# Performance work log

Measured on AMD Instinct MI355X. Metric: run time of the kernel, lower is better.

The kernel has to match this reference:

```python
import jax, jax.numpy as jnp
import numpy as np

B, T, HID = 4, 2048, 1024
H, DK, DV, K = 8, 64, 128, 4
EPS = 1e-5


def _dw_causal_conv(x, w, b):
    # x: (B,T,C), w: (C,1,K) depthwise, b: (C,). Causal: left-pad K-1.
    xt = jnp.transpose(x, (0, 2, 1))  # (B,C,T)
    y = jax.lax.conv_general_dilated(
        xt, w, window_strides=(1,), padding=[(K - 1, 0)],
        dimension_numbers=("NCH", "OIH", "NCH"), feature_group_count=x.shape[-1])
    y = y + b[None, :, None]
    return jnp.transpose(y, (0, 2, 1))  # (B,T,C)


def setup_inputs() -> dict:
    key = jax.random.key(0)
    ks = jax.random.split(key, 20)
    s = 0.02
    inp = {
        "x": jax.random.normal(ks[0], (B, T, HID), jnp.float32),
        "Wq": jax.random.normal(ks[1], (H * DK, HID), jnp.float32) * s,
        "Wk": jax.random.normal(ks[2], (H * DK, HID), jnp.float32) * s,
        "Wv": jax.random.normal(ks[3], (H * DV, HID), jnp.float32) * s,
        "Wa": jax.random.normal(ks[4], (H * DV, HID), jnp.float32) * s,
        "ba": jax.random.normal(ks[5], (H * DV,), jnp.float32) * s,
        "Wb": jax.random.normal(ks[6], (H, HID), jnp.float32) * s,
        "bb": jax.random.normal(ks[7], (H,), jnp.float32) * s,
        "Wg": jax.random.normal(ks[8], (H * DV, HID), jnp.float32) * s,
        "Wo": jax.random.normal(ks[9], (HID, H * DV), jnp.float32) * s,
        "qc_w": jax.random.normal(ks[10], (H * DK, 1, K), jnp.float32) * 0.3,
        "qc_b": jnp.zeros((H * DK,), jnp.float32),
        "kc_w": jax.random.normal(ks[11], (H * DK, 1, K), jnp.float32) * 0.3,
        "kc_b": jnp.zeros((H * DK,), jnp.float32),
        "vc_w": jax.random.normal(ks[12], (H * DV, 1, K), jnp.float32) * 0.3,
        "vc_b": jnp.zeros((H * DV,), jnp.float32),
        "ln_w": jnp.ones((DV,), jnp.float32),
        "ln_b": jnp.zeros((DV,), jnp.float32),
    }
    return inp


def _forward(x, Wq, Wk, Wv, Wa, ba, Wb, bb, Wg, Wo,
             qc_w, qc_b, kc_w, kc_b, vc_w, vc_b, ln_w, ln_b):
    b, t = x.shape[0], x.shape[1]
    scale = DK ** -0.5
    q = x @ Wq.T
    k = x @ Wk.T
    v = x @ Wv.T
    q = jax.nn.silu(_dw_causal_conv(q, qc_w, qc_b))
    k = jax.nn.silu(_dw_causal_conv(k, kc_w, kc_b))
    v = jax.nn.silu(_dw_causal_conv(v, vc_w, vc_b))
    q = q.reshape(b, t, H, DK)
    k = (k * scale).reshape(b, t, H, DK)
    v = v.reshape(b, t, H, DV)
    a = jax.nn.sigmoid(x @ Wa.T + ba).reshape(b, t, H, DV)
    beta = jax.nn.sigmoid(x @ Wb.T + bb)  # (B,T,H)

    # gated delta-rule recurrence over time; state S: (B,H,DK,DV)
    def step(S, ins):
        q_t, k_t, v_t, a_t, b_t = ins
        read = jnp.einsum("bhk,bhkv->bhv", k_t, S)          # (B,H,DV)
        err = read - v_t
        S = (a_t[:, :, None, :] * S
             - b_t[:, :, None, None] * k_t[..., None] * err[:, :, None, :])
        o_t = jnp.einsum("bhk,bhkv->bhv", q_t, S)
        return S, o_t

    to_tbh = lambda u: jnp.moveaxis(u, 1, 0)  # (T,B,H,...)
    S0 = jnp.zeros((b, H, DK, DV), x.dtype)
    _, o = jax.lax.scan(step, S0, (to_tbh(q), to_tbh(k), to_tbh(v),
                                   to_tbh(a), to_tbh(beta)))
    o = jnp.moveaxis(o, 0, 1)  # (B,T,H,DV)

    # LayerNorm over DV
    mu = jnp.mean(o, axis=-1, keepdims=True)
    var = jnp.mean((o - mu) ** 2, axis=-1, keepdims=True)
    o = (o - mu) * jax.lax.rsqrt(var + EPS) * ln_w + ln_b

    g = jax.nn.sigmoid(x @ Wg.T).reshape(b, t, H, DV)
    o = (o * g).reshape(b, t, H * DV)
    return o @ Wo.T


def reference(x, Wq, Wk, Wv, Wa, ba, Wb, bb, Wg, Wo,
              qc_w, qc_b, kc_w, kc_b, vc_w, vc_b, ln_w, ln_b):
    return _forward(x, Wq, Wk, Wv, Wa, ba, Wb, bb, Wg, Wo,
                    qc_w, qc_b, kc_w, kc_b, vc_w, vc_b, ln_w, ln_b)
```

## Files before the change

### kernel.cpp

```cpp
#include <hip/hip_runtime.h>
#include <hip/hip_bf16.h>
#include <cstdint>
#include <cstddef>

#define TDIM 2048
#define NH 8

using f32x4 = __attribute__((ext_vector_type(4))) float;
using s16x8 = __attribute__((ext_vector_type(8))) short;

__device__ __forceinline__ float sigm(float x) { return 1.0f / (1.0f + __expf(-x)); }

#define GLDS(gp, lp)                                                          \
    __builtin_amdgcn_global_load_lds(                                         \
        (const __attribute__((address_space(1))) void*)(gp),                  \
        (__attribute__((address_space(3))) void*)(lp), 16, 0, 0)
#define GLDS4(gp, lp)                                                         \
    __builtin_amdgcn_global_load_lds(                                         \
        (const __attribute__((address_space(1))) void*)(gp),                  \
        (__attribute__((address_space(3))) void*)(lp), 4, 0, 0)

template<int CTRL>
__device__ __forceinline__ float dpp_add(float x) {
    int p = __builtin_amdgcn_mov_dpp(__float_as_int(x), CTRL, 0xF, 0xF, true);
    return x + __int_as_float(p);
}
__device__ __forceinline__ float reduce16(float x) {
    x = dpp_add<0xB1>(x);
    x = dpp_add<0x4E>(x);
    x = dpp_add<0x141>(x);
    x = dpp_add<0x140>(x);
    return x;
}

__global__ __launch_bounds__(256) void pack_f32_bf16_kernel(
    const float* __restrict__ src, __hip_bfloat16* __restrict__ dst, int n4)
{
    int i = blockIdx.x * 256 + threadIdx.x;
    if (i >= n4) return;
    float4 v = *(const float4*)(src + (size_t)i * 4);
    size_t o = (size_t)i * 4;
    dst[o + 0] = __float2bfloat16(v.x);
    dst[o + 1] = __float2bfloat16(v.y);
    dst[o + 2] = __float2bfloat16(v.z);
    dst[o + 3] = __float2bfloat16(v.w);
}

__global__ __launch_bounds__(256) void pack_w_kernel(
    const float* __restrict__ Wq, const float* __restrict__ Wk,
    const float* __restrict__ Wv, const float* __restrict__ Wa,
    const float* __restrict__ Wb, const float* __restrict__ Wg,
    __hip_bfloat16* __restrict__ dst)
{
    int e = blockIdx.x * 256 + threadIdx.x;
    int r = e >> 10, c = e & 1023;
    float vv;
    if      (r <  512) vv = Wq[(size_t)r * 1024 + c];
    else if (r < 1024) vv = Wk[(size_t)(r -  512) * 1024 + c];
    else if (r < 2048) vv = Wv[(size_t)(r - 1024) * 1024 + c];
    else if (r < 3072) vv = Wa[(size_t)(r - 2048) * 1024 + c];
    else if (r < 3080) vv = Wb[(size_t)(r - 3072) * 1024 + c];
    else if (r < 4104) vv = Wg[(size_t)(r - 3080) * 1024 + c];
    else               vv = 0.0f;
    dst[e] = __float2bfloat16(vv);
}

__global__ __launch_bounds__(256) void gemm1_kernel(
    const __hip_bfloat16* __restrict__ A, const __hip_bfloat16* __restrict__ Bw,
    float* __restrict__ qraw, float* __restrict__ kraw, float* __restrict__ vraw,
    float* __restrict__ abuf, float* __restrict__ betab, float* __restrict__ gbuf,
    const float* __restrict__ ba, const float* __restrict__ bb)
{
    constexpr int Kd = 1024;
    __shared__ __attribute__((aligned(16))) __hip_bfloat16 At[128 * 32];
    __shared__ __attribute__((aligned(16))) __hip_bfloat16 Bt[128 * 32];
    __shared__ __attribute__((aligned(16))) float Ct[4][16 * 68];
    const int tid = threadIdx.x;
    const int mBase = blockIdx.x * 128;
    const int nBase = blockIdx.y * 128;
    const int wave = tid >> 6, lane = tid & 63;
    const int wm = (wave >> 1) * 64, wn = (wave & 1) * 64;
    const int quad = lane >> 4, l16 = lane & 15;

    f32x4 acc[4][4];
    for (int i = 0; i < 4; i++)
        for (int j = 0; j < 4; j++)
            for (int r = 0; r < 4; r++) acc[i][j][r] = 0.0f;

    const int srow = tid >> 2;
    const int skk = (tid & 3) * 8;
    const __hip_bfloat16* Ag = A + (size_t)(mBase + srow) * Kd + skk;
    const __hip_bfloat16* Bg = Bw + (size_t)(nBase + srow) * Kd + skk;
    __hip_bfloat16* Al = &At[srow * 32 + skk];
    __hip_bfloat16* Bl = &Bt[srow * 32 + skk];

    for (int k0 = 0; k0 < Kd; k0 += 32) {
        GLDS(Ag + k0, Al);
        GLDS(Ag + k0 + (size_t)64 * Kd, Al + 64 * 32);
        GLDS(Bg + k0, Bl);
        GLDS(Bg + k0 + (size_t)64 * Kd, Bl + 64 * 32);
        __syncthreads();
        s16x8 af[4], bfr[4];
#pragma unroll
        for (int i = 0; i < 4; i++)
            af[i] = *(const s16x8*)&At[(wm + i * 16 + l16) * 32 + quad * 8];
#pragma unroll
        for (int j = 0; j < 4; j++)
            bfr[j] = *(const s16x8*)&Bt[(wn + j * 16 + l16) * 32 + quad * 8];
#pragma unroll
        for (int i = 0; i < 4; i++)
#pragma unroll
            for (int j = 0; j < 4; j++)
                acc[i][j] = __builtin_amdgcn_mfma_f32_16x16x32_bf16(af[i], bfr[j], acc[i][j], 0, 0, 0);
        __syncthreads();
    }

    const int ncol = nBase + wn + l16 * 4;
    float* basep; size_t rstr; bool dosig = false; bool skip = false;
    float4 bias = make_float4(0.f, 0.f, 0.f, 0.f);
    if (ncol < 512)       { basep = qraw + ncol;          rstr = 512;  }
    else if (ncol < 1024) { basep = kraw + (ncol - 512);  rstr = 512;  }
    else if (ncol < 2048) { basep = vraw + (ncol - 1024); rstr = 1024; }
    else if (ncol < 3072) { basep = abuf + (ncol - 2048); rstr = 1024; dosig = true;
                            bias = *(const float4*)(ba + (ncol - 2048)); }
    else if (ncol < 3080) { basep = betab + (ncol - 3072); rstr = 8;   dosig = true;
                            bias = *(const float4*)(bb + (ncol - 3072)); }
    else if (ncol < 4104) { basep = gbuf + (ncol - 3080); rstr = 1024; dosig = true; }
    else                  { basep = gbuf; rstr = 0; skip = true; }

#pragma unroll
    for (int i = 0; i < 4; i++) {
#pragma unroll
        for (int j = 0; j < 4; j++)
#pragma unroll
            for (int r = 0; r < 4; r++)
                Ct[wave][(quad * 4 + r) * 68 + j * 16 + l16] = acc[i][j][r];
        __syncthreads();
#pragma unroll
        for (int p = 0; p < 4; p++) {
            int rr = p * 4 + quad;
            float4 val = *(const float4*)&Ct[wave][rr * 68 + l16 * 4];
            if (dosig) {
                val.x = sigm(val.x + bias.x);
                val.y = sigm(val.y + bias.y);
                val.z = sigm(val.z + bias.z);
                val.w = sigm(val.w + bias.w);
            }
            int m = mBase + wm + i * 16 + rr;
            if (!skip) *(float4*)(basep + (size_t)m * rstr) = val;
        }
        __syncthreads();
    }
}

__global__ __launch_bounds__(256) void gemm2_kernel(
    const __hip_bfloat16* __restrict__ A, const __hip_bfloat16* __restrict__ Bw,
    float* __restrict__ out)
{
    constexpr int Kd = 1024;
    __shared__ __attribute__((aligned(16))) __hip_bfloat16 At[128 * 32];
    __shared__ __attribute__((aligned(16))) __hip_bfloat16 Bt[128 * 32];
    __shared__ __attribute__((aligned(16))) float Ct[4][16 * 68];
    const int tid = threadIdx.x;
    const int mBase = blockIdx.x * 128;
    const int nBase = blockIdx.y * 128;
    const int wave = tid >> 6, lane = tid & 63;
    const int wm = (wave >> 1) * 64, wn = (wave & 1) * 64;
    const int quad = lane >> 4, l16 = lane & 15;

    f32x4 acc[4][4];
    for (int i = 0; i < 4; i++)
        for (int j = 0; j < 4; j++)
            for (int r = 0; r < 4; r++) acc[i][j][r] = 0.0f;

    const int srow = tid >> 2;
    const int skk = (tid & 3) * 8;
    const __hip_bfloat16* Ag = A + (size_t)(mBase + srow) * Kd + skk;
    const __hip_bfloat16* Bg = Bw + (size_t)(nBase + srow) * Kd + skk;
    __hip_bfloat16* Al = &At[srow * 32 + skk];
    __hip_bfloat16* Bl = &Bt[srow * 32 + skk];

    for (int k0 = 0; k0 < Kd; k0 += 32) {
        GLDS(Ag + k0, Al);
        GLDS(Ag + k0 + (size_t)64 * Kd, Al + 64 * 32);
        GLDS(Bg + k0, Bl);
        GLDS(Bg + k0 + (size_t)64 * Kd, Bl + 64 * 32);
        __syncthreads();
        s16x8 af[4], bfr[4];
#pragma unroll
        for (int i = 0; i < 4; i++)
            af[i] = *(const s16x8*)&At[(wm + i * 16 + l16) * 32 + quad * 8];
#pragma unroll
        for (int j = 0; j < 4; j++)
            bfr[j] = *(const s16x8*)&Bt[(wn + j * 16 + l16) * 32 + quad * 8];
#pragma unroll
        for (int i = 0; i < 4; i++)
#pragma unroll
            for (int j = 0; j < 4; j++)
                acc[i][j] = __builtin_amdgcn_mfma_f32_16x16x32_bf16(af[i], bfr[j], acc[i][j], 0, 0, 0);
        __syncthreads();
    }

    const int ncol = nBase + wn + l16 * 4;
    float* basep = out + ncol;
#pragma unroll
    for (int i = 0; i < 4; i++) {
#pragma unroll
        for (int j = 0; j < 4; j++)
#pragma unroll
            for (int r = 0; r < 4; r++)
                Ct[wave][(quad * 4 + r) * 68 + j * 16 + l16] = acc[i][j][r];
        __syncthreads();
#pragma unroll
        for (int p = 0; p < 4; p++) {
            int rr = p * 4 + quad;
            float4 val = *(const float4*)&Ct[wave][rr * 68 + l16 * 4];
            int m = mBase + wm + i * 16 + rr;
            *(float4*)(basep + (size_t)m * 1024) = val;
        }
        __syncthreads();
    }
}

__global__ __launch_bounds__(256) void conv_silu_fused_kernel(
    const float* __restrict__ qraw, const float* __restrict__ kraw,
    const float* __restrict__ vraw,
    const float* __restrict__ qw, const float* __restrict__ qb,
    const float* __restrict__ kw, const float* __restrict__ kb,
    const float* __restrict__ vw, const float* __restrict__ vb,
    float* __restrict__ qcb, float* __restrict__ kcb, float* __restrict__ vcb)
{
    int e = blockIdx.x * 256 + threadIdx.x;
    int c = e & 2047;
    int bt = e >> 11;
    int t = bt & (TDIM - 1);
    const float* src; float* dst; const float* w4; const float* bi;
    int C, cc; float scale = 1.0f;
    if (c < 512)       { src = qraw; dst = qcb; w4 = qw; bi = qb; C = 512;  cc = c; }
    else if (c < 1024) { src = kraw; dst = kcb; w4 = kw; bi = kb; C = 512;  cc = c - 512; scale = 0.125f; }
    else               { src = vraw; dst = vcb; w4 = vw; bi = vb; C = 1024; cc = c - 1024; }
    const float* wc = w4 + (size_t)cc * 4;
    const float* s = src + (size_t)bt * C + cc;
    float acc = bi[cc];
    acc = fmaf(s[0], wc[3], acc);
    if (t >= 1) acc = fmaf(s[-C], wc[2], acc);
    if (t >= 2) acc = fmaf(s[-2 * C], wc[1], acc);
    if (t >= 3) acc = fmaf(s[-3 * C], wc[0], acc);
    dst[(size_t)bt * C + cc] = acc * sigm(acc) * scale;
}

#define CH 32
#define NCHUNK (TDIM / CH)

#define SCAN_STAGE(BUF, T0) do {                                              \
    _Pragma("unroll") for (int j = 0; j < 8; j++) {                           \
        int flat = j * 64 + lane;                                             \
        int tt = flat >> 4, c4 = (flat & 15) * 4;                             \
        GLDS(kc + kqB + (size_t)((T0) + tt) * 512 + c4, &kL[BUF][j * 256]);   \
        GLDS(qc + kqB + (size_t)((T0) + tt) * 512 + c4, &qL[BUF][j * 256]);   \
    }                                                                         \
    _Pragma("unroll") for (int j = 0; j < 2; j++) {                           \
        int flat = j * 64 + lane;                                             \
        int tt = flat >> 2, c1 = flat & 3;                                    \
        GLDS4(vc + vaB + (size_t)((T0) + tt) * 1024 + c1, &vL[BUF][j * 64]);  \
        GLDS4(ab + vaB + (size_t)((T0) + tt) * 1024 + c1, &aL[BUF][j * 64]);  \
    }                                                                         \
    if (lane < CH)                                                            \
        GLDS4(betab + beB + (size_t)((T0) + lane) * 8, &bL[BUF][0]);          \
} while (0)

#define LOADOPS(BUF, TT, SL) do {                                             \
    kR[SL] = *(const float4*)&kL[BUF][(TT) * 64 + ks * 4];                    \
    qR[SL] = *(const float4*)&qL[BUF][(TT) * 64 + ks * 4];                    \
    vR[SL] = vL[BUF][(TT) * 4 + vi];                                          \
    aR[SL] = aL[BUF][(TT) * 4 + vi];                                          \
    bR[SL] = bL[BUF][TT];                                                     \
} while (0)

#define CSTEP(SL, TT) do {                                                    \
    const float4 kk = kR[SL];                                                 \
    const float4 qq = qR[SL];                                                 \
    const float AA = aR[SL], BB = bR[SL], VV = vR[SL];                        \
    float as0 = AA * S0, as1 = AA * S1, as2 = AA * S2, as3 = AA * S3;         \
    float bv = BB * VV;                                                       \
    float r0 = kk.x * S0, r1 = kk.y * S1;                                     \
    r0 = fmaf(kk.z, S2, r0); r1 = fmaf(kk.w, S3, r1);                         \
    float rr = reduce16(r0 + r1);                                             \
    float cc = fmaf(BB, rr, -bv);                                             \
    S0 = fmaf(-cc, kk.x, as0); float o0 = qq.x * S0;                          \
    S1 = fmaf(-cc, kk.y, as1); float o1 = qq.y * S1;                          \
    S2 = fmaf(-cc, kk.z, as2); o0 = fmaf(qq.z, S2, o0);                       \
    S3 = fmaf(-cc, kk.w, as3); o1 = fmaf(qq.w, S3, o1);                       \
    oacc[TT] = reduce16(o0 + o1);                                             \
} while (0)

__global__ __launch_bounds__(64) void scan_kernel(
    const float* __restrict__ qc, const float* __restrict__ kc,
    const float* __restrict__ vc, const float* __restrict__ ab,
    const float* __restrict__ betab, float* __restrict__ ob)
{
    __shared__ __attribute__((aligned(16))) float kL[2][CH * 64];
    __shared__ __attribute__((aligned(16))) float qL[2][CH * 64];
    __shared__ __attribute__((aligned(16))) float vL[2][CH * 4];
    __shared__ __attribute__((aligned(16))) float aL[2][CH * 4];
    __shared__ __attribute__((aligned(16))) float bL[2][CH];
    __shared__ __attribute__((aligned(16))) float oL[4 * CH];

    const int bid = blockIdx.x;
    const int bh = bid & 31, vg = bid >> 5;
    const int h = bh & 7, b = bh >> 3;
    const int lane = threadIdx.x;
    const int ks = lane & 15, vi = lane >> 4;

    const size_t kqB = (size_t)b * TDIM * 512 + (size_t)h * 64;
    const size_t vaB = (size_t)b * TDIM * 1024 + (size_t)h * 128 + (size_t)vg * 4;
    const size_t beB = (size_t)b * TDIM * 8 + h;

    float S0 = 0, S1 = 0, S2 = 0, S3 = 0;
    float4 kR[4], qR[4];
    float vR[4], aR[4], bR[4];
    float oacc[CH];

    SCAN_STAGE(0, 0);
    __syncthreads();
    LOADOPS(0, 0, 0); LOADOPS(0, 1, 1); LOADOPS(0, 2, 2); LOADOPS(0, 3, 3);

    for (int chk = 0; chk < NCHUNK; chk++) {
        const int buf = chk & 1;
        const int nb = buf ^ 1;
        const int tn = (chk + 1 < NCHUNK) ? (chk + 1) * CH : 0;
        SCAN_STAGE(nb, tn);
#pragma unroll
        for (int t = 0; t < CH; t++) {
            CSTEP(t & 3, t);
            if (t + 4 < CH) LOADOPS(buf, t + 4, t & 3);
        }
        if (ks == 0) {
#pragma unroll
            for (int j = 0; j < 8; j++) {
                float4 o4 = make_float4(oacc[j * 4], oacc[j * 4 + 1],
                                        oacc[j * 4 + 2], oacc[j * 4 + 3]);
                *(float4*)&oL[vi * CH + j * 4] = o4;
            }
        }
        __syncthreads();
        if (lane < CH) {
            float4 ov = make_float4(oL[0 * CH + lane], oL[1 * CH + lane],
                                    oL[2 * CH + lane], oL[3 * CH + lane]);
            *(float4*)(ob + vaB + (size_t)(chk * CH + lane) * 1024) = ov;
        }
        LOADOPS(nb, 0, 0); LOADOPS(nb, 1, 1); LOADOPS(nb, 2, 2); LOADOPS(nb, 3, 3);
    }
}

__global__ __launch_bounds__(256) void ln_gate_kernel(
    const float* __restrict__ ob, const float* __restrict__ g,
    const float* __restrict__ lnw, const float* __restrict__ lnb,
    __hip_bfloat16* __restrict__ opr)
{
    int row = blockIdx.x * 4 + (threadIdx.x >> 6);
    int lane = threadIdx.x & 63;
    size_t base = (size_t)row * 128 + lane * 2;
    float2 xv = *(const float2*)(ob + base);
    float s = xv.x + xv.y;
#pragma unroll
    for (int m = 1; m <= 32; m <<= 1) s += __shfl_xor(s, m);
    float mean = s * (1.0f / 128.0f);
    float d0 = xv.x - mean, d1 = xv.y - mean;
    float vs = d0 * d0 + d1 * d1;
#pragma unroll
    for (int m = 1; m <= 32; m <<= 1) vs += __shfl_xor(vs, m);
    float rstd = rsqrtf(vs * (1.0f / 128.0f) + 1e-5f);
    float2 gv = *(const float2*)(g + base);
    float w0 = lnw[lane * 2], w1 = lnw[lane * 2 + 1];
    float b0 = lnb[lane * 2], b1 = lnb[lane * 2 + 1];
    opr[base] = __float2bfloat16((d0 * rstd * w0 + b0) * gv.x);
    opr[base + 1] = __float2bfloat16((d1 * rstd * w1 + b1) * gv.y);
}

extern "C" void kernel_launch(void* const* d_in, const int* in_sizes, int n_in,
                              void* d_out, int out_size, void* d_ws, size_t ws_size,
                              hipStream_t stream)
{
    const float* x    = (const float*)d_in[0];
    const float* Wq   = (const float*)d_in[1];
    const float* Wk   = (const float*)d_in[2];
    const float* Wv   = (const float*)d_in[3];
    const float* Wa   = (const float*)d_in[4];
    const float* ba   = (const float*)d_in[5];
    const float* Wb   = (const float*)d_in[6];
    const float* bb   = (const float*)d_in[7];
    const float* Wg   = (const float*)d_in[8];
    const float* Wo   = (const float*)d_in[9];
    const float* qc_w = (const float*)d_in[10];
    const float* qc_b = (const float*)d_in[11];
    const float* kc_w = (const float*)d_in[12];
    const float* kc_b = (const float*)d_in[13];
    const float* vc_w = (const float*)d_in[14];
    const float* vc_b = (const float*)d_in[15];
    const float* ln_w = (const float*)d_in[16];
    const float* ln_b = (const float*)d_in[17];
    float* out = (float*)d_out;

    char* W = (char*)d_ws;
    __hip_bfloat16* xbf  = (__hip_bfloat16*)(W + 0);
    __hip_bfloat16* wcat = (__hip_bfloat16*)(W + 16777216);
    __hip_bfloat16* wobf = (__hip_bfloat16*)(W + 25427968);
    float* qraw  = (float*)(W + 27525120);
    float* kraw  = (float*)(W + 44302336);
    float* vraw  = (float*)(W + 61079552);
    float* abuf  = (float*)(W + 94633984);
    float* betab = (float*)(W + 128188416);
    float* gbuf  = (float*)(W + 128450560);
    float* kcb   = (float*)(W + 162004992);
    float* vcb   = (float*)(W + 178782208);
    float* qcb   = (float*)xbf;
    float* obuf  = (float*)qraw;
    __hip_bfloat16* opr = (__hip_bfloat16*)vraw;

    pack_f32_bf16_kernel<<<8192, 256, 0, stream>>>(x, xbf, 2097152);
    pack_w_kernel<<<16896, 256, 0, stream>>>(Wq, Wk, Wv, Wa, Wb, Wg, wcat);
    pack_f32_bf16_kernel<<<1024, 256, 0, stream>>>(Wo, wobf, 262144);
    gemm1_kernel<<<dim3(64, 33), 256, 0, stream>>>(xbf, wcat, qraw, kraw, vraw,
                                                   abuf, betab, gbuf, ba, bb);
    conv_silu_fused_kernel<<<65536, 256, 0, stream>>>(
        qraw, kraw, vraw, qc_w, qc_b, kc_w, kc_b, vc_w, vc_b, qcb, kcb, vcb);
    scan_kernel<<<1024, 64, 0, stream>>>(qcb, kcb, vcb, abuf, betab, obuf);
    ln_gate_kernel<<<16384, 256, 0, stream>>>(obuf, gbuf, ln_w, ln_b, opr);
    gemm2_kernel<<<dim3(64, 8), 256, 0, stream>>>(opr, wobf, out);
}
```

Measured before the change: 596.0 us.

## Process two value columns per lane in scan kernel using packed f32x2 math

Each scan lane now owns two DV columns instead of one, so the grid halves from 1024 to 512 wavefronts and the k/q loads and reductions are amortized over twice the state. The state update uses two-wide float vectors that can map to packed FMA instructions on MI355X, and both DPP reductions operate on pairs. Output accumulation switches from a 32-entry register array to two per-lane registers selected by timestep, which lowers register pressure. The trade-off is fewer wavefronts to hide the latency of the serial recurrence, with each step carrying more dependent work.

```diff
diff --git a/kernel.cpp b/kernel.cpp
--- a/kernel.cpp
+++ b/kernel.cpp
@@ -6,6 +6,7 @@
 #define TDIM 2048
 #define NH 8
 
+using f32x2 = __attribute__((ext_vector_type(2))) float;
 using f32x4 = __attribute__((ext_vector_type(4))) float;
 using s16x8 = __attribute__((ext_vector_type(8))) short;
 
@@ -21,16 +22,25 @@
         (__attribute__((address_space(3))) void*)(lp), 4, 0, 0)
 
 template<int CTRL>
-__device__ __forceinline__ float dpp_add(float x) {
-    int p = __builtin_amdgcn_mov_dpp(__float_as_int(x), CTRL, 0xF, 0xF, true);
-    return x + __int_as_float(p);
-}
-__device__ __forceinline__ float reduce16(float x) {
-    x = dpp_add<0xB1>(x);
-    x = dpp_add<0x4E>(x);
-    x = dpp_add<0x141>(x);
-    x = dpp_add<0x140>(x);
+__device__ __forceinline__ f32x2 dpp_add2(f32x2 x) {
+    int px = __builtin_amdgcn_mov_dpp(__float_as_int(x[0]), CTRL, 0xF, 0xF, true);
+    int py = __builtin_amdgcn_mov_dpp(__float_as_int(x[1]), CTRL, 0xF, 0xF, true);
+    f32x2 p;
+    p[0] = __int_as_float(px);
+    p[1] = __int_as_float(py);
+    return x + p;
+}
+__device__ __forceinline__ f32x2 reduce16_2(f32x2 x) {
+    x = dpp_add2<0xB1>(x);
+    x = dpp_add2<0x4E>(x);
+    x = dpp_add2<0x141>(x);
+    x = dpp_add2<0x140>(x);
     return x;
+}
+
+__device__ __forceinline__ f32x2 splat2(float s) { f32x2 r; r[0] = s; r[1] = s; return r; }
+__device__ __forceinline__ f32x2 fma2(f32x2 a, f32x2 b, f32x2 c) {
+    return __builtin_elementwise_fma(a, b, c);
 }
 
 __global__ __launch_bounds__(256) void pack_f32_bf16_kernel(
@@ -259,39 +269,41 @@
         GLDS(kc + kqB + (size_t)((T0) + tt) * 512 + c4, &kL[BUF][j * 256]);   \
         GLDS(qc + kqB + (size_t)((T0) + tt) * 512 + c4, &qL[BUF][j * 256]);   \
     }                                                                         \
-    _Pragma("unroll") for (int j = 0; j < 2; j++) {                           \
-        int flat = j * 64 + lane;                                             \
-        int tt = flat >> 2, c1 = flat & 3;                                    \
-        GLDS4(vc + vaB + (size_t)((T0) + tt) * 1024 + c1, &vL[BUF][j * 64]);  \
-        GLDS4(ab + vaB + (size_t)((T0) + tt) * 1024 + c1, &aL[BUF][j * 64]);  \
+    {                                                                         \
+        int tt = lane >> 1, c4 = (lane & 1) * 4;                              \
+        GLDS(vc + vaB + (size_t)((T0) + tt) * 1024 + c4, &vL[BUF][0]);        \
+        GLDS(ab + vaB + (size_t)((T0) + tt) * 1024 + c4, &aL[BUF][0]);        \
     }                                                                         \
     if (lane < CH)                                                            \
         GLDS4(betab + beB + (size_t)((T0) + lane) * 8, &bL[BUF][0]);          \
 } while (0)
 
 #define LOADOPS(BUF, TT, SL) do {                                             \
-    kR[SL] = *(const float4*)&kL[BUF][(TT) * 64 + ks * 4];                    \
-    qR[SL] = *(const float4*)&qL[BUF][(TT) * 64 + ks * 4];                    \
-    vR[SL] = vL[BUF][(TT) * 4 + vi];                                          \
-    aR[SL] = aL[BUF][(TT) * 4 + vi];                                          \
+    kR[SL] = *(const f32x4*)&kL[BUF][(TT) * 64 + ks * 4];                     \
+    qR[SL] = *(const f32x4*)&qL[BUF][(TT) * 64 + ks * 4];                     \
+    vR[SL] = *(const f32x2*)&vL[BUF][(TT) * 8 + vi * 2];                      \
+    aR[SL] = *(const f32x2*)&aL[BUF][(TT) * 8 + vi * 2];                      \
     bR[SL] = bL[BUF][TT];                                                     \
 } while (0)
 
 #define CSTEP(SL, TT) do {                                                    \
-    const float4 kk = kR[SL];                                                 \
-    const float4 qq = qR[SL];                                                 \
-    const float AA = aR[SL], BB = bR[SL], VV = vR[SL];                        \
-    float as0 = AA * S0, as1 = AA * S1, as2 = AA * S2, as3 = AA * S3;         \
-    float bv = BB * VV;                                                       \
-    float r0 = kk.x * S0, r1 = kk.y * S1;                                     \
-    r0 = fmaf(kk.z, S2, r0); r1 = fmaf(kk.w, S3, r1);                         \
-    float rr = reduce16(r0 + r1);                                             \
-    float cc = fmaf(BB, rr, -bv);                                             \
-    S0 = fmaf(-cc, kk.x, as0); float o0 = qq.x * S0;                          \
-    S1 = fmaf(-cc, kk.y, as1); float o1 = qq.y * S1;                          \
-    S2 = fmaf(-cc, kk.z, as2); o0 = fmaf(qq.z, S2, o0);                       \
-    S3 = fmaf(-cc, kk.w, as3); o1 = fmaf(qq.w, S3, o1);                       \
-    oacc[TT] = reduce16(o0 + o1);                                             \
+    const f32x4 kk = kR[SL];                                                  \
+    const f32x4 qq = qR[SL];                                                  \
+    const f32x2 AA = aR[SL], VV = vR[SL];                                     \
+    const float BB = bR[SL];                                                  \
+    f32x2 as0 = AA * S0, as1 = AA * S1, as2 = AA * S2, as3 = AA * S3;         \
+    f32x2 nbv = VV * (-BB);                                                   \
+    f32x2 r0 = S0 * kk.x, r1 = S1 * kk.y;                                     \
+    r0 = fma2(S2, splat2(kk.z), r0); r1 = fma2(S3, splat2(kk.w), r1);         \
+    f32x2 rr = reduce16_2(r0 + r1);                                           \
+    f32x2 cc = fma2(rr, splat2(BB), nbv);                                     \
+    f32x2 ncc = -cc;                                                          \
+    S0 = fma2(ncc, splat2(kk.x), as0); f32x2 o0 = S0 * qq.x;                  \
+    S1 = fma2(ncc, splat2(kk.y), as1); f32x2 o1 = S1 * qq.y;                  \
+    S2 = fma2(ncc, splat2(kk.z), as2); o0 = fma2(S2, splat2(qq.z), o0);       \
+    S3 = fma2(ncc, splat2(kk.w), as3); o1 = fma2(S3, splat2(qq.w), o1);       \
+    f32x2 oo = reduce16_2(o0 + o1);                                           \
+    if (ks == ((TT) & 15)) { if ((TT) < 16) oA = oo; else oB = oo; }          \
 } while (0)
 
 __global__ __launch_bounds__(64) void scan_kernel(
@@ -301,10 +313,10 @@
 {
     __shared__ __attribute__((aligned(16))) float kL[2][CH * 64];
     __shared__ __attribute__((aligned(16))) float qL[2][CH * 64];
-    __shared__ __attribute__((aligned(16))) float vL[2][CH * 4];
-    __shared__ __attribute__((aligned(16))) float aL[2][CH * 4];
+    __shared__ __attribute__((aligned(16))) float vL[2][CH * 8];
+    __shared__ __attribute__((aligned(16))) float aL[2][CH * 8];
     __shared__ __attribute__((aligned(16))) float bL[2][CH];
-    __shared__ __attribute__((aligned(16))) float oL[4 * CH];
+    __shared__ __attribute__((aligned(16))) float oL[CH * 8];
 
     const int bid = blockIdx.x;
     const int bh = bid & 31, vg = bid >> 5;
@@ -313,13 +325,14 @@
     const int ks = lane & 15, vi = lane >> 4;
 
     const size_t kqB = (size_t)b * TDIM * 512 + (size_t)h * 64;
-    const size_t vaB = (size_t)b * TDIM * 1024 + (size_t)h * 128 + (size_t)vg * 4;
+    const size_t vaB = (size_t)b * TDIM * 1024 + (size_t)h * 128 + (size_t)vg * 8;
     const size_t beB = (size_t)b * TDIM * 8 + h;
 
-    float S0 = 0, S1 = 0, S2 = 0, S3 = 0;
-    float4 kR[4], qR[4];
-    float vR[4], aR[4], bR[4];
-    float oacc[CH];
+    f32x2 S0 = splat2(0.f), S1 = splat2(0.f), S2 = splat2(0.f), S3 = splat2(0.f);
+    f32x4 kR[4], qR[4];
+    f32x2 vR[4], aR[4];
+    float bR[4];
+    f32x2 oA = splat2(0.f), oB = splat2(0.f);
 
     SCAN_STAGE(0, 0);
     __syncthreads();
@@ -335,19 +348,15 @@
             CSTEP(t & 3, t);
             if (t + 4 < CH) LOADOPS(buf, t + 4, t & 3);
         }
-        if (ks == 0) {
-#pragma unroll
-            for (int j = 0; j < 8; j++) {
-                float4 o4 = make_float4(oacc[j * 4], oacc[j * 4 + 1],
-                                        oacc[j * 4 + 2], oacc[j * 4 + 3]);
-                *(float4*)&oL[vi * CH + j * 4] = o4;
-            }
-        }
+        *(f32x2*)&oL[ks * 8 + vi * 2] = oA;
+        *(f32x2*)&oL[(ks + 16) * 8 + vi * 2] = oB;
         __syncthreads();
         if (lane < CH) {
-            float4 ov = make_float4(oL[0 * CH + lane], oL[1 * CH + lane],
-                                    oL[2 * CH + lane], oL[3 * CH + lane]);
-            *(float4*)(ob + vaB + (size_t)(chk * CH + lane) * 1024) = ov;
+            f32x4 lo = *(const f32x4*)&oL[lane * 8];
+            f32x4 hi = *(const f32x4*)&oL[lane * 8 + 4];
+            size_t rbase = vaB + (size_t)(chk * CH + lane) * 1024;
+            *(f32x4*)(ob + rbase) = lo;
+            *(f32x4*)(ob + rbase + 4) = hi;
         }
         LOADOPS(nb, 0, 0); LOADOPS(nb, 1, 1); LOADOPS(nb, 2, 2); LOADOPS(nb, 3, 3);
     }
@@ -425,7 +434,7 @@
                                                    abuf, betab, gbuf, ba, bb);
     conv_silu_fused_kernel<<<65536, 256, 0, stream>>>(
         qraw, kraw, vraw, qc_w, qc_b, kc_w, kc_b, vc_w, vc_b, qcb, kcb, vcb);
-    scan_kernel<<<1024, 64, 0, stream>>>(qcb, kcb, vcb, abuf, betab, obuf);
+    scan_kernel<<<512, 64, 0, stream>>>(qcb, kcb, vcb, abuf, betab, obuf);
     ln_gate_kernel<<<16384, 256, 0, stream>>>(obuf, gbuf, ln_w, ln_b, opr);
     gemm2_kernel<<<dim3(64, 8), 256, 0, stream>>>(opr, wobf, out);
 }
```

After: 656.8 us. 1.1x slower.

## Process two scan timesteps per iteration using Gram-term algebra to batch reductions

Applied to the files above, without the earlier changes.

Rewrites the delta-rule recurrence step so two consecutive timesteps are computed together. All dot products needed for both steps (k and q against the old state, plus the k1·k2, q·k cross terms) are formed from the pre-update state. Their eight cross-lane reductions are therefore independent and can overlap, instead of four serially dependent reductions. The aim is to shorten the latency-bound dependency chain of the scan. In exchange it does more FMAs and reductions per pair, and the expanded algebra rounds slightly differently in float32.

```diff
diff --git a/kernel.cpp b/kernel.cpp
--- a/kernel.cpp
+++ b/kernel.cpp
@@ -277,21 +277,41 @@
     bR[SL] = bL[BUF][TT];                                                     \
 } while (0)
 
-#define CSTEP(SL, TT) do {                                                    \
-    const float4 kk = kR[SL];                                                 \
-    const float4 qq = qR[SL];                                                 \
-    const float AA = aR[SL], BB = bR[SL], VV = vR[SL];                        \
-    float as0 = AA * S0, as1 = AA * S1, as2 = AA * S2, as3 = AA * S3;         \
-    float bv = BB * VV;                                                       \
-    float r0 = kk.x * S0, r1 = kk.y * S1;                                     \
-    r0 = fmaf(kk.z, S2, r0); r1 = fmaf(kk.w, S3, r1);                         \
-    float rr = reduce16(r0 + r1);                                             \
-    float cc = fmaf(BB, rr, -bv);                                             \
-    S0 = fmaf(-cc, kk.x, as0); float o0 = qq.x * S0;                          \
-    S1 = fmaf(-cc, kk.y, as1); float o1 = qq.y * S1;                          \
-    S2 = fmaf(-cc, kk.z, as2); o0 = fmaf(qq.z, S2, o0);                       \
-    S3 = fmaf(-cc, kk.w, as3); o1 = fmaf(qq.w, S3, o1);                       \
-    oacc[TT] = reduce16(o0 + o1);                                             \
+#define CPAIR(SLA, SLB, TA) do {                                              \
+    const float4 k1 = kR[SLA], q1 = qR[SLA];                                  \
+    const float4 k2 = kR[SLB], q2 = qR[SLB];                                  \
+    const float A1 = aR[SLA], V1 = vR[SLA], B1 = bR[SLA];                     \
+    const float A2 = aR[SLB], V2 = vR[SLB], B2 = bR[SLB];                     \
+    float u1 = k1.x * S0, u2 = k2.x * S0, w1 = q1.x * S0, w2 = q2.x * S0;     \
+    u1 = fmaf(k1.y, S1, u1); u2 = fmaf(k2.y, S1, u2);                         \
+    w1 = fmaf(q1.y, S1, w1); w2 = fmaf(q2.y, S1, w2);                         \
+    u1 = fmaf(k1.z, S2, u1); u2 = fmaf(k2.z, S2, u2);                         \
+    w1 = fmaf(q1.z, S2, w1); w2 = fmaf(q2.z, S2, w2);                         \
+    u1 = fmaf(k1.w, S3, u1); u2 = fmaf(k2.w, S3, u2);                         \
+    w1 = fmaf(q1.w, S3, w1); w2 = fmaf(q2.w, S3, w2);                         \
+    float g21 = k2.x * k1.x, h11 = q1.x * k1.x;                               \
+    float h21 = q2.x * k1.x, h22 = q2.x * k2.x;                               \
+    g21 = fmaf(k2.y, k1.y, g21); h11 = fmaf(q1.y, k1.y, h11);                 \
+    h21 = fmaf(q2.y, k1.y, h21); h22 = fmaf(q2.y, k2.y, h22);                 \
+    g21 = fmaf(k2.z, k1.z, g21); h11 = fmaf(q1.z, k1.z, h11);                 \
+    h21 = fmaf(q2.z, k1.z, h21); h22 = fmaf(q2.z, k2.z, h22);                 \
+    g21 = fmaf(k2.w, k1.w, g21); h11 = fmaf(q1.w, k1.w, h11);                 \
+    h21 = fmaf(q2.w, k1.w, h21); h22 = fmaf(q2.w, k2.w, h22);                 \
+    u1 = reduce16(u1); u2 = reduce16(u2);                                     \
+    w1 = reduce16(w1); w2 = reduce16(w2);                                     \
+    g21 = reduce16(g21); h11 = reduce16(h11);                                 \
+    h21 = reduce16(h21); h22 = reduce16(h22);                                 \
+    const float c1 = B1 * (u1 - V1);                                          \
+    const float r2 = fmaf(A1, u2, -(c1 * g21));                               \
+    const float c2 = B2 * (r2 - V2);                                          \
+    oacc[TA] = fmaf(A1, w1, -(c1 * h11));                                     \
+    const float o2p = fmaf(A1, w2, -(c1 * h21));                              \
+    oacc[(TA) + 1] = fmaf(A2, o2p, -(c2 * h22));                              \
+    float tu;                                                                 \
+    tu = fmaf(-c1, k1.x, A1 * S0); S0 = fmaf(-c2, k2.x, A2 * tu);             \
+    tu = fmaf(-c1, k1.y, A1 * S1); S1 = fmaf(-c2, k2.y, A2 * tu);             \
+    tu = fmaf(-c1, k1.z, A1 * S2); S2 = fmaf(-c2, k2.z, A2 * tu);             \
+    tu = fmaf(-c1, k1.w, A1 * S3); S3 = fmaf(-c2, k2.w, A2 * tu);             \
 } while (0)
 
 __global__ __launch_bounds__(64) void scan_kernel(
@@ -331,9 +351,12 @@
         const int tn = (chk + 1 < NCHUNK) ? (chk + 1) * CH : 0;
         SCAN_STAGE(nb, tn);
 #pragma unroll
-        for (int t = 0; t < CH; t++) {
-            CSTEP(t & 3, t);
-            if (t + 4 < CH) LOADOPS(buf, t + 4, t & 3);
+        for (int t = 0; t < CH; t += 2) {
+            CPAIR(t & 3, (t + 1) & 3, t);
+            if (t + 4 < CH) {
+                LOADOPS(buf, t + 4, t & 3);
+                LOADOPS(buf, t + 5, (t + 1) & 3);
+            }
         }
         if (ks == 0) {
 #pragma unroll
```

Result: slower. 674.2 us (+13.1%).

## Compute four timesteps per conv thread and pack v/a/beta into one LDS float4

Applied to the files above, without the earlier changes.

The causal conv kernel now has each thread produce four consecutive timesteps from seven loaded inputs, cutting redundant neighbor loads and launching a quarter of the blocks. The scan kernel stops using three separate scalar global-to-LDS transfers for v, a and beta. It loads them into registers ahead of the chunk's compute, then writes them interleaved as one float4 per (t, v) into LDS, so each step needs a single vector LDS read. This trades async LDS DMA for register-held prefetches and regular LDS stores, which adds register pressure and global-load latency in the scan loop.

```diff
diff --git a/kernel.cpp b/kernel.cpp
--- a/kernel.cpp
+++ b/kernel.cpp
@@ -232,61 +232,62 @@
 {
     int e = blockIdx.x * 256 + threadIdx.x;
     int c = e & 2047;
-    int bt = e >> 11;
-    int t = bt & (TDIM - 1);
+    int bt4 = e >> 11;
+    int t0 = (bt4 & 511) * 4;
+    int bb_ = bt4 >> 9;
     const float* src; float* dst; const float* w4; const float* bi;
     int C, cc; float scale = 1.0f;
     if (c < 512)       { src = qraw; dst = qcb; w4 = qw; bi = qb; C = 512;  cc = c; }
     else if (c < 1024) { src = kraw; dst = kcb; w4 = kw; bi = kb; C = 512;  cc = c - 512; scale = 0.125f; }
     else               { src = vraw; dst = vcb; w4 = vw; bi = vb; C = 1024; cc = c - 1024; }
     const float* wc = w4 + (size_t)cc * 4;
-    const float* s = src + (size_t)bt * C + cc;
-    float acc = bi[cc];
-    acc = fmaf(s[0], wc[3], acc);
-    if (t >= 1) acc = fmaf(s[-C], wc[2], acc);
-    if (t >= 2) acc = fmaf(s[-2 * C], wc[1], acc);
-    if (t >= 3) acc = fmaf(s[-3 * C], wc[0], acc);
-    dst[(size_t)bt * C + cc] = acc * sigm(acc) * scale;
+    const float w0 = wc[0], w1 = wc[1], w2 = wc[2], w3 = wc[3];
+    const float bs = bi[cc];
+    const float* s = src + ((size_t)bb_ * TDIM + t0) * C + cc;
+    float x0, x1, x2;
+    if (t0 == 0) { x0 = 0.f; x1 = 0.f; x2 = 0.f; }
+    else { x0 = s[-3 * C]; x1 = s[-2 * C]; x2 = s[-C]; }
+    const float x3 = s[0], x4 = s[C], x5 = s[2 * C], x6 = s[3 * C];
+    float* d = dst + ((size_t)bb_ * TDIM + t0) * C + cc;
+    float y;
+    y = fmaf(w0, x0, fmaf(w1, x1, fmaf(w2, x2, fmaf(w3, x3, bs))));
+    d[0] = y * sigm(y) * scale;
+    y = fmaf(w0, x1, fmaf(w1, x2, fmaf(w2, x3, fmaf(w3, x4, bs))));
+    d[C] = y * sigm(y) * scale;
+    y = fmaf(w0, x2, fmaf(w1, x3, fmaf(w2, x4, fmaf(w3, x5, bs))));
+    d[2 * C] = y * sigm(y) * scale;
+    y = fmaf(w0, x3, fmaf(w1, x4, fmaf(w2, x5, fmaf(w3, x6, bs))));
+    d[3 * C] = y * sigm(y) * scale;
 }
 
 #define CH 32
 #define NCHUNK (TDIM / CH)
 
-#define SCAN_STAGE(BUF, T0) do {                                              \
+#define SCAN_STAGE_KQ(BUF, T0) do {                                           \
     _Pragma("unroll") for (int j = 0; j < 8; j++) {                           \
         int flat = j * 64 + lane;                                             \
         int tt = flat >> 4, c4 = (flat & 15) * 4;                             \
         GLDS(kc + kqB + (size_t)((T0) + tt) * 512 + c4, &kL[BUF][j * 256]);   \
         GLDS(qc + kqB + (size_t)((T0) + tt) * 512 + c4, &qL[BUF][j * 256]);   \
     }                                                                         \
-    _Pragma("unroll") for (int j = 0; j < 2; j++) {                           \
-        int flat = j * 64 + lane;                                             \
-        int tt = flat >> 2, c1 = flat & 3;                                    \
-        GLDS4(vc + vaB + (size_t)((T0) + tt) * 1024 + c1, &vL[BUF][j * 64]);  \
-        GLDS4(ab + vaB + (size_t)((T0) + tt) * 1024 + c1, &aL[BUF][j * 64]);  \
-    }                                                                         \
-    if (lane < CH)                                                            \
-        GLDS4(betab + beB + (size_t)((T0) + lane) * 8, &bL[BUF][0]);          \
 } while (0)
 
 #define LOADOPS(BUF, TT, SL) do {                                             \
     kR[SL] = *(const float4*)&kL[BUF][(TT) * 64 + ks * 4];                    \
     qR[SL] = *(const float4*)&qL[BUF][(TT) * 64 + ks * 4];                    \
-    vR[SL] = vL[BUF][(TT) * 4 + vi];                                          \
-    aR[SL] = aL[BUF][(TT) * 4 + vi];                                          \
-    bR[SL] = bL[BUF][TT];                                                     \
+    vabR[SL] = *(const float4*)&vabL[BUF][((TT) * 4 + vi) * 4];               \
 } while (0)
 
 #define CSTEP(SL, TT) do {                                                    \
     const float4 kk = kR[SL];                                                 \
     const float4 qq = qR[SL];                                                 \
-    const float AA = aR[SL], BB = bR[SL], VV = vR[SL];                        \
+    const float VV = vabR[SL].x, AA = vabR[SL].y, BB = vabR[SL].z;            \
     float as0 = AA * S0, as1 = AA * S1, as2 = AA * S2, as3 = AA * S3;         \
-    float bv = BB * VV;                                                       \
+    float nbv = VV * (-BB);                                                   \
     float r0 = kk.x * S0, r1 = kk.y * S1;                                     \
     r0 = fmaf(kk.z, S2, r0); r1 = fmaf(kk.w, S3, r1);                         \
     float rr = reduce16(r0 + r1);                                             \
-    float cc = fmaf(BB, rr, -bv);                                             \
+    float cc = fmaf(BB, rr, nbv);                                             \
     S0 = fmaf(-cc, kk.x, as0); float o0 = qq.x * S0;                          \
     S1 = fmaf(-cc, kk.y, as1); float o1 = qq.y * S1;                          \
     S2 = fmaf(-cc, kk.z, as2); o0 = fmaf(qq.z, S2, o0);                       \
@@ -301,9 +302,7 @@
 {
     __shared__ __attribute__((aligned(16))) float kL[2][CH * 64];
     __shared__ __attribute__((aligned(16))) float qL[2][CH * 64];
-    __shared__ __attribute__((aligned(16))) float vL[2][CH * 4];
-    __shared__ __attribute__((aligned(16))) float aL[2][CH * 4];
-    __shared__ __attribute__((aligned(16))) float bL[2][CH];
+    __shared__ __attribute__((aligned(16))) float vabL[2][CH * 4 * 4];
     __shared__ __attribute__((aligned(16))) float oL[4 * CH];
 
     const int bid = blockIdx.x;
@@ -316,12 +315,24 @@
     const size_t vaB = (size_t)b * TDIM * 1024 + (size_t)h * 128 + (size_t)vg * 4;
     const size_t beB = (size_t)b * TDIM * 8 + h;
 
+    const int t0p = lane >> 2, c0p = lane & 3;
+    const int t1p = 16 + t0p;
+
     float S0 = 0, S1 = 0, S2 = 0, S3 = 0;
-    float4 kR[4], qR[4];
-    float vR[4], aR[4], bR[4];
+    float4 kR[4], qR[4], vabR[4];
     float oacc[CH];
 
-    SCAN_STAGE(0, 0);
+    SCAN_STAGE_KQ(0, 0);
+    {
+        float v0 = vc[vaB + (size_t)t0p * 1024 + c0p];
+        float a0 = ab[vaB + (size_t)t0p * 1024 + c0p];
+        float e0 = betab[beB + (size_t)t0p * 8];
+        float v1 = vc[vaB + (size_t)t1p * 1024 + c0p];
+        float a1 = ab[vaB + (size_t)t1p * 1024 + c0p];
+        float e1 = betab[beB + (size_t)t1p * 8];
+        *(float4*)&vabL[0][lane * 4] = make_float4(v0, a0, e0, 0.f);
+        *(float4*)&vabL[0][(64 + lane) * 4] = make_float4(v1, a1, e1, 0.f);
+    }
     __syncthreads();
     LOADOPS(0, 0, 0); LOADOPS(0, 1, 1); LOADOPS(0, 2, 2); LOADOPS(0, 3, 3);
 
@@ -329,12 +340,20 @@
         const int buf = chk & 1;
         const int nb = buf ^ 1;
         const int tn = (chk + 1 < NCHUNK) ? (chk + 1) * CH : 0;
-        SCAN_STAGE(nb, tn);
+        SCAN_STAGE_KQ(nb, tn);
+        const float nv0 = vc[vaB + (size_t)(tn + t0p) * 1024 + c0p];
+        const float na0 = ab[vaB + (size_t)(tn + t0p) * 1024 + c0p];
+        const float ne0 = betab[beB + (size_t)(tn + t0p) * 8];
+        const float nv1 = vc[vaB + (size_t)(tn + t1p) * 1024 + c0p];
+        const float na1 = ab[vaB + (size_t)(tn + t1p) * 1024 + c0p];
+        const float ne1 = betab[beB + (size_t)(tn + t1p) * 8];
 #pragma unroll
         for (int t = 0; t < CH; t++) {
             CSTEP(t & 3, t);
             if (t + 4 < CH) LOADOPS(buf, t + 4, t & 3);
         }
+        *(float4*)&vabL[nb][lane * 4] = make_float4(nv0, na0, ne0, 0.f);
+        *(float4*)&vabL[nb][(64 + lane) * 4] = make_float4(nv1, na1, ne1, 0.f);
         if (ks == 0) {
 #pragma unroll
             for (int j = 0; j < 8; j++) {
@@ -423,7 +442,7 @@
     pack_f32_bf16_kernel<<<1024, 256, 0, stream>>>(Wo, wobf, 262144);
     gemm1_kernel<<<dim3(64, 33), 256, 0, stream>>>(xbf, wcat, qraw, kraw, vraw,
                                                    abuf, betab, gbuf, ba, bb);
-    conv_silu_fused_kernel<<<65536, 256, 0, stream>>>(
+    conv_silu_fused_kernel<<<16384, 256, 0, stream>>>(
         qraw, kraw, vraw, qc_w, qc_b, kc_w, kc_b, vc_w, vc_b, qcb, kcb, vcb);
     scan_kernel<<<1024, 64, 0, stream>>>(qcb, kcb, vcb, abuf, betab, obuf);
     ln_gate_kernel<<<16384, 256, 0, stream>>>(obuf, gbuf, ln_w, ln_b, opr);
```

New measurement: 536.2 us. 1.11x faster.
